# Kernel optimization log

Hardware: AMD Instinct MI355X
Metric: run time of the kernel (lower is better)

## Reference

```python
import jax, jax.numpy as jnp
import numpy as np


def conv1x1(x, W, b):
    # 1x1 Conv2d == per-pixel linear over channels. x: [B,C,H,W], W: [O,C], b: [O]
    return jnp.einsum('oc,bchw->bohw', W, x) + b[None, :, None, None]


def setup_inputs() -> dict:
    key = jax.random.key(0)
    ks = jax.random.split(key, 18)
    B, C, Hd, H, W = 16, 64, 64, 32, 32
    s = 0.05
    f = jax.random.normal
    return {
        'h': f(ks[0], (B, C, H, W), jnp.float32),
        'm': f(ks[1], (B, C, H, W), jnp.float32),
        'Wq': f(ks[2], (Hd, C), jnp.float32) * s,
        'bq': f(ks[3], (Hd,), jnp.float32) * s,
        'Wk': f(ks[4], (Hd, C), jnp.float32) * s,
        'bk': f(ks[5], (Hd,), jnp.float32) * s,
        'Wk2': f(ks[6], (Hd, C), jnp.float32) * s,
        'bk2': f(ks[7], (Hd,), jnp.float32) * s,
        'Wv': f(ks[8], (C, C), jnp.float32) * s,
        'bv': f(ks[9], (C,), jnp.float32) * s,
        'Wv2': f(ks[10], (C, C), jnp.float32) * s,
        'bv2': f(ks[11], (C,), jnp.float32) * s,
        'Wz': f(ks[12], (2 * C, 2 * C), jnp.float32) * s,
        'bz': f(ks[13], (2 * C,), jnp.float32) * s,
        'Wm': f(ks[14], (3 * C, 3 * C), jnp.float32) * s,
        'bm': f(ks[15], (3 * C,), jnp.float32) * s,
    }


def reference(h, m, Wq, bq, Wk, bk, Wk2, bk2, Wv, bv, Wv2, bv2, Wz, bz, Wm, bm):
    B, C, H, W = h.shape
    Hd = Wq.shape[0]
    N = H * W
    # Shared query from h
    Q_h = conv1x1(h, Wq, bq).reshape(B, Hd, N).transpose(0, 2, 1)  # [B,N,Hd]
    # Self-attention branch over h
    K_h = conv1x1(h, Wk, bk).reshape(B, Hd, N)                     # [B,Hd,N]
    A_h = jax.nn.softmax(jnp.einsum('bnd,bdm->bnm', Q_h, K_h), axis=-1)  # [B,N,N]
    V_h = conv1x1(h, Wv, bv).reshape(B, C, N)                      # [B,C,N]
    Z_h = jnp.einsum('bnm,bcm->bcn', A_h, V_h).reshape(B, C, H, W)
    # Cross-attention branch over memory m (same query Q_h)
    K_m = conv1x1(m, Wk2, bk2).reshape(B, Hd, N)
    A_m = jax.nn.softmax(jnp.einsum('bnd,bdm->bnm', Q_h, K_m), axis=-1)
    V_m = conv1x1(m, Wv2, bv2).reshape(B, C, N)
    Z_m = jnp.einsum('bnm,bcm->bcn', A_m, V_m).reshape(B, C, H, W)
    # Fuse and gated memory update
    Z = conv1x1(jnp.concatenate([Z_h, Z_m], axis=1), Wz, bz)       # [B,2C,H,W]
    combined = conv1x1(jnp.concatenate([Z, h], axis=1), Wm, bm)    # [B,3C,H,W]
    mo, mg, mi = combined[:, :C], combined[:, C:2 * C], combined[:, 2 * C:]
    mi = jax.nn.sigmoid(mi)
    new_m = (1 - mi) * m + mi * jnp.tanh(mg)
    new_h = jax.nn.sigmoid(mo) * new_m
    return (new_h, new_m)
```

## Files before the change

### kernel.cpp

```cpp
#include <hip/hip_runtime.h>

typedef unsigned short u16;
typedef unsigned int u32;
typedef __attribute__((ext_vector_type(8))) short bf16x8;
typedef __attribute__((ext_vector_type(4))) short bf16x4;
typedef __attribute__((ext_vector_type(4))) float f32x4;

#define MFMA(a, b, c) __builtin_amdgcn_mfma_f32_16x16x32_bf16((a), (b), (c), 0, 0, 0)
#define MFMA16(a, b, c) __builtin_amdgcn_mfma_f32_16x16x16bf16_1k((a), (b), (c), 0, 0, 0)

static __device__ __forceinline__ u16 f2bf(float x) {
  u32 u = __float_as_uint(x);
  u += 0x7FFFu + ((u >> 16) & 1u);
  return (u16)(u >> 16);
}
static __device__ __forceinline__ u32 packbf_t(float hi, float lo) {
  return __builtin_amdgcn_perm(__float_as_uint(hi), __float_as_uint(lo), 0x07060302u);
}
static __device__ __forceinline__ u32 packbf(float lo, float hi) {
  return (u32)f2bf(lo) | ((u32)f2bf(hi) << 16);
}

__global__ __launch_bounds__(256) void proj_kernel(
    const float* __restrict__ h, const float* __restrict__ m_,
    const float* __restrict__ bq, const float* __restrict__ bk,
    const float* __restrict__ bk2, const float* __restrict__ bv,
    const float* __restrict__ bv2,
    const float* __restrict__ Wq, const float* __restrict__ Wk,
    const float* __restrict__ Wk2, const float* __restrict__ Wv,
    const float* __restrict__ Wv2,
    const float* __restrict__ Wz, const float* __restrict__ Wm,
    const float* __restrict__ bm,
    u16* __restrict__ Qb, u16* __restrict__ Khb, u16* __restrict__ Kmb,
    u16* __restrict__ Vhb, u16* __restrict__ Vmb, u16* __restrict__ hbuf,
    u16* __restrict__ Wzb, u16* __restrict__ Wmb, float* __restrict__ bmp)
{
  const int tid = threadIdx.x;
  const int b = blockIdx.y, n0 = blockIdx.x * 64, z = blockIdx.z;

  {
    const int gid = (blockIdx.z * 256 + blockIdx.y * 16 + blockIdx.x) * 256 + tid;
    if (gid < 16384) {
      Wzb[gid] = f2bf(Wz[gid]);
    } else if (gid < 53248) {
      const int e = gid - 16384;
      const int p = e / 192, k = e % 192;
      const int hb2 = p / 96, r1 = p % 96, ctl = r1 / 48, r2 = r1 % 48;
      const int g = r2 >> 4, mm = r2 & 15;
      const int o = g * 64 + (hb2 * 2 + ctl) * 16 + mm;
      Wmb[p * 192 + k] = f2bf(Wm[o * 192 + k]);
    } else if (gid < 53440) {
      const int p = gid - 53248;
      const int hb2 = p / 96, r1 = p % 96, ctl = r1 / 48, r2 = r1 % 48;
      const int g = r2 >> 4, mm = r2 & 15;
      const int o = g * 64 + (hb2 * 2 + ctl) * 16 + mm;
      bmp[p] = bm[o];
    }
  }

  __shared__ __align__(16) u16 xt[64][72];
  const float* __restrict__ X = (z >= 3) ? m_ : h;

  {
    const int px = tid & 63, c0 = (tid >> 6) * 16;
#pragma unroll
    for (int i = 0; i < 8; ++i) {
      const int c = c0 + 2 * i;
      const float f0 = X[(b * 64 + c) * 1024 + n0 + px];
      const float f1 = X[(b * 64 + c + 1) * 1024 + n0 + px];
      *(u32*)&xt[px][c] = packbf(f0, f1);
    }
  }
  __syncthreads();

  const int lane = tid & 63, w = tid >> 6;
  const int mm = lane & 15, q = lane >> 4;

  const bf16x8 xa0 = *(const bf16x8*)&xt[w * 16 + mm][q * 8];
  const bf16x8 xa1 = *(const bf16x8*)&xt[w * 16 + mm][32 + q * 8];

  auto ldw8 = [&](const float* Wf, int row, int col0) {
    const float4 a = *(const float4*)(Wf + row * 64 + col0);
    const float4 bb = *(const float4*)(Wf + row * 64 + col0 + 4);
    union { u32 u[4]; bf16x8 v; } r;
    r.u[0] = packbf(a.x, a.y);
    r.u[1] = packbf(a.z, a.w);
    r.u[2] = packbf(bb.x, bb.y);
    r.u[3] = packbf(bb.z, bb.w);
    return r.v;
  };

  auto qk_store = [&](u16* dst, const float* Wf, const float* bias) {
#pragma unroll
    for (int ot = 0; ot < 4; ++ot) {
      const bf16x8 wb0 = ldw8(Wf, ot * 16 + mm, q * 8);
      const bf16x8 wb1 = ldw8(Wf, ot * 16 + mm, 32 + q * 8);
      const float4 b4 = *(const float4*)(bias + ot * 16 + q * 4);
      f32x4 d = {b4.x, b4.y, b4.z, b4.w};
      d = MFMA(wb0, xa0, d);
      d = MFMA(wb1, xa1, d);
      uint2 val;
      val.x = packbf(d[0], d[1]);
      val.y = packbf(d[2], d[3]);
      *(uint2*)(dst + (b * 1024 + n0 + w * 16 + mm) * 64 + ot * 16 + q * 4) = val;
    }
  };
  auto v_store = [&](u16* dst, const float* Wf, const float* bias) {
#pragma unroll
    for (int ot = 0; ot < 4; ++ot) {
      const bf16x8 wb0 = ldw8(Wf, ot * 16 + mm, q * 8);
      const bf16x8 wb1 = ldw8(Wf, ot * 16 + mm, 32 + q * 8);
      const float bb = bias[ot * 16 + mm];
      f32x4 d = {bb, bb, bb, bb};
      d = MFMA(xa0, wb0, d);
      d = MFMA(xa1, wb1, d);
      uint2 val;
      val.x = packbf(d[0], d[1]);
      val.y = packbf(d[2], d[3]);
      *(uint2*)(dst + b * 65536 + blockIdx.x * 4096 + w * 1024 +
                (ot * 16 + mm) * 16 + q * 4) = val;
    }
  };

  if (z == 0) {
    qk_store(Qb, Wq, bq);
    const int px = tid >> 2, sg = tid & 3;
    u32* dst = (u32*)(hbuf + (b * 1024 + n0 + px) * 64 + sg * 16);
    const u16* srcr = &xt[px][sg * 16];
#pragma unroll
    for (int j = 0; j < 8; ++j) dst[j] = *(const u32*)(srcr + 2 * j);
  } else if (z == 1) {
    qk_store(Khb, Wk, bk);
  } else if (z == 2) {
    v_store(Vhb, Wv, bv);
  } else if (z == 3) {
    qk_store(Kmb, Wk2, bk2);
  } else {
    v_store(Vmb, Wv2, bv2);
  }
}

__global__ __launch_bounds__(256) void attn_tail_kernel(
    const u16* __restrict__ Qb, const u16* __restrict__ Khb,
    const u16* __restrict__ Kmb, const u16* __restrict__ Vhb,
    const u16* __restrict__ Vmb, const u16* __restrict__ hbuf,
    const float* __restrict__ m_, const u16* __restrict__ Wzb,
    const float* __restrict__ bz, const u16* __restrict__ Wmb,
    const float* __restrict__ bmp, float* __restrict__ out)
{
  const int id = blockIdx.x;
  const int b = id & 15;
  const int qg = id >> 4;
  const int q0 = qg * 32;

  const u16* __restrict__ Kh = Khb + b * 65536;
  const u16* __restrict__ Vh = Vhb + b * 65536;
  const u16* __restrict__ Km = Kmb + b * 65536;
  const u16* __restrict__ Vm = Vmb + b * 65536;

  __shared__ __align__(16) u16 pool[21504];
  __shared__ __align__(16) u16 zp[32][136];
  __shared__ float rsw[4][32];

  const int tid = threadIdx.x, w = tid >> 6, lane = tid & 63;
  const int mm = lane & 15, q = lane >> 4;

  u16* const arenaH = pool + w * 5376;
  u16* const arenaM = arenaH + 2688;

  bf16x8 qb0[2], qb1[2];
#pragma unroll
  for (int qt = 0; qt < 2; ++qt) {
    const u16* Qp = Qb + (b * 1024 + q0 + qt * 16 + mm) * 64;
    qb0[qt] = *(const bf16x8*)(Qp + q * 8);
    qb1[qt] = *(const bf16x8*)(Qp + 32 + q * 8);
  }

  f32x4 zA[2][4], zB[2][4];
  float rpA[2] = {0.f, 0.f}, rpB[2] = {0.f, 0.f};
#pragma unroll
  for (int qt = 0; qt < 2; ++qt)
#pragma unroll
    for (int ct = 0; ct < 4; ++ct) {
      zA[qt][ct] = (f32x4){0.f, 0.f, 0.f, 0.f};
      zB[qt][ct] = (f32x4){0.f, 0.f, 0.f, 0.f};
    }

  uint4 kh0, kh1, vh0, vh1, km0, km1, vm0, vm1;
  auto ldg = [&](const u16* K, const u16* V, int kc, uint4& r0, uint4& r1,
                 uint4& s0, uint4& s1) {
    const u16* Ks = K + kc * 4096 + w * 1024 + lane * 16;
    const u16* Vs = V + kc * 4096 + w * 1024 + lane * 16;
    r0 = *(const uint4*)Ks;
    r1 = *(const uint4*)(Ks + 8);
    s0 = *(const uint4*)Vs;
    s1 = *(const uint4*)(Vs + 8);
  };
  auto stl = [&](u16* arena, const uint4& r0, const uint4& r1, const uint4& s0,
                 const uint4& s1) {
    u16* Kd = arena + (lane >> 2) * 72 + (lane & 3) * 16;
    u16* Vd = arena + 1152 + lane * 24;
    *(uint4*)Kd = r0;
    *(uint4*)(Kd + 8) = r1;
    *(uint4*)Vd = s0;
    *(uint4*)(Vd + 8) = s1;
  };

  auto compute = [&](const u16* arena, f32x4 (&z)[2][4], float (&rp)[2]) {
    const u16* Kt = arena;
    const u16* Vt = arena + 1152;
    const bf16x8 kf0 = *(const bf16x8*)(Kt + mm * 72 + q * 8);
    const bf16x8 kf1 = *(const bf16x8*)(Kt + mm * 72 + 32 + q * 8);
    bf16x4 vf[4];
#pragma unroll
    for (int ct = 0; ct < 4; ++ct)
      vf[ct] = *(const bf16x4*)(Vt + (ct * 16 + mm) * 24 + q * 4);

#pragma unroll
    for (int qt = 0; qt < 2; ++qt) {
      f32x4 s = {0.f, 0.f, 0.f, 0.f};
      s = MFMA(kf0, qb0[qt], s);
      s = MFMA(kf1, qb1[qt], s);
      const float e0 = __expf(s[0]), e1 = __expf(s[1]);
      const float e2 = __expf(s[2]), e3 = __expf(s[3]);
      rp[qt] += (e0 + e1) + (e2 + e3);
      union { u32 u[2]; bf16x4 v; } pb;
      pb.u[0] = packbf_t(e1, e0);
      pb.u[1] = packbf_t(e3, e2);
#pragma unroll
      for (int ct = 0; ct < 4; ++ct) z[qt][ct] = MFMA16(vf[ct], pb.v, z[qt][ct]);
    }
  };

  ldg(Kh, Vh, 0, kh0, kh1, vh0, vh1);
  stl(arenaH, kh0, kh1, vh0, vh1);
  ldg(Km, Vm, 0, km0, km1, vm0, vm1);
  stl(arenaM, km0, km1, vm0, vm1);
  ldg(Kh, Vh, 1, kh0, kh1, vh0, vh1);
  ldg(Km, Vm, 1, km0, km1, vm0, vm1);

#pragma unroll 1
  for (int kc = 0; kc < 16; ++kc) {
    compute(arenaH, zA, rpA);
    if (kc < 15) {
      stl(arenaH, kh0, kh1, vh0, vh1);
      if (kc < 14) ldg(Kh, Vh, kc + 2, kh0, kh1, vh0, vh1);
    }
    compute(arenaM, zB, rpB);
    if (kc < 15) {
      stl(arenaM, km0, km1, vm0, vm1);
      if (kc < 14) ldg(Km, Vm, kc + 2, km0, km1, vm0, vm1);
    }
  }

  __syncthreads();

  u16* const zcb = pool;
  auto combine = [&](int br, f32x4 (&z)[2][4], float (&rp)[2]) {
#pragma unroll
    for (int qt = 0; qt < 2; ++qt) {
      float v = rp[qt];
      v += __shfl_xor(v, 16);
      v += __shfl_xor(v, 32);
      if (q == 0) rsw[w][qt * 16 + mm] = v;
#pragma unroll
      for (int ct = 0; ct < 4; ++ct) {
        uint2 val;
        val.x = packbf_t(z[qt][ct][1], z[qt][ct][0]);
        val.y = packbf_t(z[qt][ct][3], z[qt][ct][2]);
        *(uint2*)(zcb + w * 2176 + (qt * 16 + mm) * 68 + ct * 16 + q * 4) = val;
      }
    }
    __syncthreads();
    const int c2 = tid & 31, qr = tid >> 5;
#pragma unroll
    for (int i = 0; i < 4; ++i) {
      const int query = qr + i * 8;
      const float rt = rsw[0][query] + rsw[1][query] + rsw[2][query] + rsw[3][query];
      const float rinv = __builtin_amdgcn_rcpf(rt);
      float vlo = 0.f, vhi = 0.f;
#pragma unroll
      for (int ww = 0; ww < 4; ++ww) {
        const u32 u = *(const u32*)(zcb + ww * 2176 + query * 68 + c2 * 2);
        vlo += __uint_as_float(u << 16);
        vhi += __uint_as_float(u & 0xffff0000u);
      }
      vlo *= rinv;
      vhi *= rinv;
      *(u32*)&zp[query][br * 64 + c2 * 2] = packbf_t(vhi, vlo);
    }
    __syncthreads();
  };
  combine(0, zA, rpA);
  combine(1, zB, rpB);

  const int pxt = w & 1, oh = w >> 1;
  u16* const zp2 = pool;
  {
    bf16x8 za[4];
#pragma unroll
    for (int ks = 0; ks < 4; ++ks)
      za[ks] = *(const bf16x8*)&zp[pxt * 16 + mm][ks * 32 + q * 8];
#pragma unroll
    for (int ot = 0; ot < 4; ++ot) {
      const int o0 = oh * 64 + ot * 16;
      const float4 b4 = *(const float4*)(bz + o0 + q * 4);
      f32x4 d = {b4.x, b4.y, b4.z, b4.w};
#pragma unroll
      for (int ks = 0; ks < 4; ++ks) {
        const bf16x8 wb = *(const bf16x8*)(Wzb + (o0 + mm) * 128 + ks * 32 + q * 8);
        d = MFMA(wb, za[ks], d);
      }
      uint2 val;
      val.x = packbf(d[0], d[1]);
      val.y = packbf(d[2], d[3]);
      *(uint2*)(zp2 + (pxt * 16 + mm) * 136 + o0 + q * 4) = val;
    }
  }
  __syncthreads();

  {
    const int hb2 = oh;
    bf16x8 fa[6];
#pragma unroll
    for (int ks = 0; ks < 4; ++ks)
      fa[ks] = *(const bf16x8*)(zp2 + (pxt * 16 + mm) * 136 + ks * 32 + q * 8);
    {
      const u16* hp = hbuf + (b * 1024 + q0 + pxt * 16 + mm) * 64;
      fa[4] = *(const bf16x8*)(hp + q * 8);
      fa[5] = *(const bf16x8*)(hp + 32 + q * 8);
    }
    f32x4 dd[6];
#pragma unroll
    for (int j = 0; j < 6; ++j) {
      const int p = hb2 * 96 + j * 16 + mm;
      const float bb = bmp[p];
      f32x4 d = {bb, bb, bb, bb};
#pragma unroll
      for (int ks = 0; ks < 6; ++ks) {
        const bf16x8 wb = *(const bf16x8*)(Wmb + p * 192 + ks * 32 + q * 8);
        d = MFMA(fa[ks], wb, d);
      }
      dd[j] = d;
    }
#pragma unroll
    for (int ctl = 0; ctl < 2; ++ctl) {
      const int c = (hb2 * 2 + ctl) * 16 + mm;
      const int px = q0 + pxt * 16 + q * 4;
      const float4 mold = *(const float4*)(m_ + (b * 64 + c) * 1024 + px);
      float4 nh, nm;
#pragma unroll
      for (int r = 0; r < 4; ++r) {
        const float xo = dd[ctl * 3 + 0][r];
        const float xg = dd[ctl * 3 + 1][r];
        const float xi = dd[ctl * 3 + 2][r];
        const float si = __builtin_amdgcn_rcpf(1.f + __expf(-xi));
        const float th = 1.f - 2.f * __builtin_amdgcn_rcpf(__expf(2.f * xg) + 1.f);
        const float so = __builtin_amdgcn_rcpf(1.f + __expf(-xo));
        const float mo = ((const float*)&mold)[r];
        const float nmv = (1.f - si) * mo + si * th;
        ((float*)&nm)[r] = nmv;
        ((float*)&nh)[r] = so * nmv;
      }
      *(float4*)(out + (b * 64 + c) * 1024 + px) = nh;
      *(float4*)(out + 1048576 + (b * 64 + c) * 1024 + px) = nm;
    }
  }
}

extern "C" void kernel_launch(void* const* d_in, const int* in_sizes, int n_in,
                              void* d_out, int out_size, void* d_ws, size_t ws_size,
                              hipStream_t stream) {
  const float* h   = (const float*)d_in[0];
  const float* m   = (const float*)d_in[1];
  const float* Wq  = (const float*)d_in[2];
  const float* bq  = (const float*)d_in[3];
  const float* Wk  = (const float*)d_in[4];
  const float* bk  = (const float*)d_in[5];
  const float* Wk2 = (const float*)d_in[6];
  const float* bk2 = (const float*)d_in[7];
  const float* Wv  = (const float*)d_in[8];
  const float* bv  = (const float*)d_in[9];
  const float* Wv2 = (const float*)d_in[10];
  const float* bv2 = (const float*)d_in[11];
  const float* Wz  = (const float*)d_in[12];
  const float* bz  = (const float*)d_in[13];
  const float* Wm  = (const float*)d_in[14];
  const float* bm  = (const float*)d_in[15];
  float* out = (float*)d_out;

  char* ws = (char*)d_ws;
  const size_t MB = 1024 * 1024;
  u16* Qb   = (u16*)(ws + 0 * MB);
  u16* Khb  = (u16*)(ws + 2 * MB);
  u16* Kmb  = (u16*)(ws + 4 * MB);
  u16* Vhb  = (u16*)(ws + 6 * MB);
  u16* Vmb  = (u16*)(ws + 8 * MB);
  u16* hbuf = (u16*)(ws + 10 * MB);
  u16* Wzb  = (u16*)(ws + 16 * MB + 40960);
  u16* Wmb  = (u16*)(ws + 16 * MB + 73728);
  float* bmp = (float*)(ws + 16 * MB + 147456);

  proj_kernel<<<dim3(16, 16, 5), 256, 0, stream>>>(
      h, m, bq, bk, bk2, bv, bv2, Wq, Wk, Wk2, Wv, Wv2, Wz, Wm, bm,
      Qb, Khb, Kmb, Vhb, Vmb, hbuf, Wzb, Wmb, bmp);
  attn_tail_kernel<<<512, 256, 0, stream>>>(Qb, Khb, Kmb, Vhb, Vmb, hbuf, m,
                                            Wzb, bz, Wmb, bmp, out);
}
```

Measured before the change: 133.5 us.

## Fold log2e into projection weights, use raw exp2, interleave both attention branches

Scales the Q projection and the gated-update weights and biases by log2(e) (and 2·log2(e) for the tanh gate) when the weights are precomputed. The softmax and activations can then call the hardware v_exp_f32 directly instead of __expf, which saves a multiply per exponential. The self and cross attention branches are also computed in one interleaved step, so their MFMA chains are independent and can overlap, and the K/V LDS stores and global loads for both branches are grouped together. This may raise register pressure and changes bf16 rounding slightly because scaling happens before conversion.

Result: no change. 135.1 us (+1.1%).

```diff
diff --git a/kernel.cpp b/kernel.cpp
--- a/kernel.cpp
+++ b/kernel.cpp
@@ -8,6 +8,14 @@
 
 #define MFMA(a, b, c) __builtin_amdgcn_mfma_f32_16x16x32_bf16((a), (b), (c), 0, 0, 0)
 #define MFMA16(a, b, c) __builtin_amdgcn_mfma_f32_16x16x16bf16_1k((a), (b), (c), 0, 0, 0)
+
+#define LOG2E 1.442695041f
+
+static __device__ __forceinline__ float ex2(float x) {
+  float r;
+  asm("v_exp_f32 %0, %1" : "=v"(r) : "v"(x));
+  return r;
+}
 
 static __device__ __forceinline__ u16 f2bf(float x) {
   u32 u = __float_as_uint(x);
@@ -48,13 +56,15 @@
       const int hb2 = p / 96, r1 = p % 96, ctl = r1 / 48, r2 = r1 % 48;
       const int g = r2 >> 4, mm = r2 & 15;
       const int o = g * 64 + (hb2 * 2 + ctl) * 16 + mm;
-      Wmb[p * 192 + k] = f2bf(Wm[o * 192 + k]);
+      const float scl = (g == 1) ? 2.f * LOG2E : LOG2E;
+      Wmb[p * 192 + k] = f2bf(Wm[o * 192 + k] * scl);
     } else if (gid < 53440) {
       const int p = gid - 53248;
       const int hb2 = p / 96, r1 = p % 96, ctl = r1 / 48, r2 = r1 % 48;
       const int g = r2 >> 4, mm = r2 & 15;
       const int o = g * 64 + (hb2 * 2 + ctl) * 16 + mm;
-      bmp[p] = bm[o];
+      const float scl = (g == 1) ? 2.f * LOG2E : LOG2E;
+      bmp[p] = bm[o] * scl;
     }
   }
 
@@ -79,24 +89,24 @@
   const bf16x8 xa0 = *(const bf16x8*)&xt[w * 16 + mm][q * 8];
   const bf16x8 xa1 = *(const bf16x8*)&xt[w * 16 + mm][32 + q * 8];
 
-  auto ldw8 = [&](const float* Wf, int row, int col0) {
+  auto ldw8 = [&](const float* Wf, int row, int col0, float scl) {
     const float4 a = *(const float4*)(Wf + row * 64 + col0);
     const float4 bb = *(const float4*)(Wf + row * 64 + col0 + 4);
     union { u32 u[4]; bf16x8 v; } r;
-    r.u[0] = packbf(a.x, a.y);
-    r.u[1] = packbf(a.z, a.w);
-    r.u[2] = packbf(bb.x, bb.y);
-    r.u[3] = packbf(bb.z, bb.w);
+    r.u[0] = packbf(a.x * scl, a.y * scl);
+    r.u[1] = packbf(a.z * scl, a.w * scl);
+    r.u[2] = packbf(bb.x * scl, bb.y * scl);
+    r.u[3] = packbf(bb.z * scl, bb.w * scl);
     return r.v;
   };
 
-  auto qk_store = [&](u16* dst, const float* Wf, const float* bias) {
+  auto qk_store = [&](u16* dst, const float* Wf, const float* bias, float scl) {
 #pragma unroll
     for (int ot = 0; ot < 4; ++ot) {
-      const bf16x8 wb0 = ldw8(Wf, ot * 16 + mm, q * 8);
-      const bf16x8 wb1 = ldw8(Wf, ot * 16 + mm, 32 + q * 8);
+      const bf16x8 wb0 = ldw8(Wf, ot * 16 + mm, q * 8, scl);
+      const bf16x8 wb1 = ldw8(Wf, ot * 16 + mm, 32 + q * 8, scl);
       const float4 b4 = *(const float4*)(bias + ot * 16 + q * 4);
-      f32x4 d = {b4.x, b4.y, b4.z, b4.w};
+      f32x4 d = {b4.x * scl, b4.y * scl, b4.z * scl, b4.w * scl};
       d = MFMA(wb0, xa0, d);
       d = MFMA(wb1, xa1, d);
       uint2 val;
@@ -108,8 +118,8 @@
   auto v_store = [&](u16* dst, const float* Wf, const float* bias) {
 #pragma unroll
     for (int ot = 0; ot < 4; ++ot) {
-      const bf16x8 wb0 = ldw8(Wf, ot * 16 + mm, q * 8);
-      const bf16x8 wb1 = ldw8(Wf, ot * 16 + mm, 32 + q * 8);
+      const bf16x8 wb0 = ldw8(Wf, ot * 16 + mm, q * 8, 1.f);
+      const bf16x8 wb1 = ldw8(Wf, ot * 16 + mm, 32 + q * 8, 1.f);
       const float bb = bias[ot * 16 + mm];
       f32x4 d = {bb, bb, bb, bb};
       d = MFMA(xa0, wb0, d);
@@ -123,18 +133,18 @@
   };
 
   if (z == 0) {
-    qk_store(Qb, Wq, bq);
+    qk_store(Qb, Wq, bq, LOG2E);
     const int px = tid >> 2, sg = tid & 3;
     u32* dst = (u32*)(hbuf + (b * 1024 + n0 + px) * 64 + sg * 16);
     const u16* srcr = &xt[px][sg * 16];
 #pragma unroll
     for (int j = 0; j < 8; ++j) dst[j] = *(const u32*)(srcr + 2 * j);
   } else if (z == 1) {
-    qk_store(Khb, Wk, bk);
+    qk_store(Khb, Wk, bk, 1.f);
   } else if (z == 2) {
     v_store(Vhb, Wv, bv);
   } else if (z == 3) {
-    qk_store(Kmb, Wk2, bk2);
+    qk_store(Kmb, Wk2, bk2, 1.f);
   } else {
     v_store(Vmb, Wv2, bv2);
   }
@@ -206,30 +216,36 @@
     *(uint4*)(Vd + 8) = s1;
   };
 
-  auto compute = [&](const u16* arena, f32x4 (&z)[2][4], float (&rp)[2]) {
-    const u16* Kt = arena;
-    const u16* Vt = arena + 1152;
-    const bf16x8 kf0 = *(const bf16x8*)(Kt + mm * 72 + q * 8);
-    const bf16x8 kf1 = *(const bf16x8*)(Kt + mm * 72 + 32 + q * 8);
-    bf16x4 vf[4];
-#pragma unroll
-    for (int ct = 0; ct < 4; ++ct)
-      vf[ct] = *(const bf16x4*)(Vt + (ct * 16 + mm) * 24 + q * 4);
-
-#pragma unroll
-    for (int qt = 0; qt < 2; ++qt) {
-      f32x4 s = {0.f, 0.f, 0.f, 0.f};
-      s = MFMA(kf0, qb0[qt], s);
-      s = MFMA(kf1, qb1[qt], s);
-      const float e0 = __expf(s[0]), e1 = __expf(s[1]);
-      const float e2 = __expf(s[2]), e3 = __expf(s[3]);
-      rp[qt] += (e0 + e1) + (e2 + e3);
-      union { u32 u[2]; bf16x4 v; } pb;
-      pb.u[0] = packbf_t(e1, e0);
-      pb.u[1] = packbf_t(e3, e2);
-#pragma unroll
-      for (int ct = 0; ct < 4; ++ct) z[qt][ct] = MFMA16(vf[ct], pb.v, z[qt][ct]);
-    }
+  auto chain = [&](const bf16x8& kf0, const bf16x8& kf1, const bf16x4* vf,
+                   int qt, f32x4 (&z)[2][4], float (&rp)[2]) {
+    f32x4 s = {0.f, 0.f, 0.f, 0.f};
+    s = MFMA(kf0, qb0[qt], s);
+    s = MFMA(kf1, qb1[qt], s);
+    const float e0 = ex2(s[0]), e1 = ex2(s[1]);
+    const float e2 = ex2(s[2]), e3 = ex2(s[3]);
+    rp[qt] += (e0 + e1) + (e2 + e3);
+    union { u32 u[2]; bf16x4 v; } pb;
+    pb.u[0] = packbf_t(e1, e0);
+    pb.u[1] = packbf_t(e3, e2);
+#pragma unroll
+    for (int ct = 0; ct < 4; ++ct) z[qt][ct] = MFMA16(vf[ct], pb.v, z[qt][ct]);
+  };
+
+  auto compute_both = [&]() {
+    const bf16x8 kfH0 = *(const bf16x8*)(arenaH + mm * 72 + q * 8);
+    const bf16x8 kfH1 = *(const bf16x8*)(arenaH + mm * 72 + 32 + q * 8);
+    const bf16x8 kfM0 = *(const bf16x8*)(arenaM + mm * 72 + q * 8);
+    const bf16x8 kfM1 = *(const bf16x8*)(arenaM + mm * 72 + 32 + q * 8);
+    bf16x4 vfH[4], vfM[4];
+#pragma unroll
+    for (int ct = 0; ct < 4; ++ct) {
+      vfH[ct] = *(const bf16x4*)(arenaH + 1152 + (ct * 16 + mm) * 24 + q * 4);
+      vfM[ct] = *(const bf16x4*)(arenaM + 1152 + (ct * 16 + mm) * 24 + q * 4);
+    }
+    chain(kfH0, kfH1, vfH, 0, zA, rpA);
+    chain(kfM0, kfM1, vfM, 0, zB, rpB);
+    chain(kfH0, kfH1, vfH, 1, zA, rpA);
+    chain(kfM0, kfM1, vfM, 1, zB, rpB);
   };
 
   ldg(Kh, Vh, 0, kh0, kh1, vh0, vh1);
@@ -241,15 +257,14 @@
 
 #pragma unroll 1
   for (int kc = 0; kc < 16; ++kc) {
-    compute(arenaH, zA, rpA);
+    compute_both();
     if (kc < 15) {
       stl(arenaH, kh0, kh1, vh0, vh1);
-      if (kc < 14) ldg(Kh, Vh, kc + 2, kh0, kh1, vh0, vh1);
-    }
-    compute(arenaM, zB, rpB);
-    if (kc < 15) {
       stl(arenaM, km0, km1, vm0, vm1);
-      if (kc < 14) ldg(Km, Vm, kc + 2, km0, km1, vm0, vm1);
+      if (kc < 14) {
+        ldg(Kh, Vh, kc + 2, kh0, kh1, vh0, vh1);
+        ldg(Km, Vm, kc + 2, km0, km1, vm0, vm1);
+      }
     }
   }
 
@@ -354,9 +369,9 @@
         const float xo = dd[ctl * 3 + 0][r];
         const float xg = dd[ctl * 3 + 1][r];
         const float xi = dd[ctl * 3 + 2][r];
-        const float si = __builtin_amdgcn_rcpf(1.f + __expf(-xi));
-        const float th = 1.f - 2.f * __builtin_amdgcn_rcpf(__expf(2.f * xg) + 1.f);
-        const float so = __builtin_amdgcn_rcpf(1.f + __expf(-xo));
+        const float si = __builtin_amdgcn_rcpf(1.f + ex2(-xi));
+        const float th = 1.f - 2.f * __builtin_amdgcn_rcpf(ex2(xg) + 1.f);
+        const float so = __builtin_amdgcn_rcpf(1.f + ex2(-xo));
         const float mo = ((const float*)&mold)[r];
         const float nmv = (1.f - si) * mo + si * th;
         ((float*)&nm)[r] = nmv;
```
